# Performance work log

Measured on AMD Instinct MI355X. Metric: run time of the kernel, lower is better.

## Reference

```python
import jax, jax.numpy as jnp
import numpy as np

# H36M 17-joint skeleton: parent-of array
_PARENTS = [-1, 0, 1, 2, 0, 4, 5, 0, 7, 8, 9, 8, 11, 12, 8, 14, 15]

def _make_triplets():
    # (jp, j, jc) for every joint j with a parent jp and child jc
    trips = []
    for jc, j in enumerate(_PARENTS):
        if j <= 0 and j != 0:
            continue
        if j == -1:
            continue
        jp = _PARENTS[j]
        if jp == -1:
            continue
        trips.append((jp, j, jc))
    return trips

TRIPLETS = _make_triplets()  # 12 fixed triplets

B, N, J, C = 16, 243, 17, 512
H, D = 8, C // 8
EPS = 1e-5


def setup_inputs() -> dict:
    key = jax.random.key(0)
    ks = jax.random.split(key, 5)
    s = 1.0 / np.sqrt(C)
    x = jax.random.normal(ks[0], (B, N, J, C), dtype=jnp.float32)
    Wqkv = jax.random.normal(ks[1], (C, 3 * C), dtype=jnp.float32) * s
    bqkv = jax.random.normal(ks[2], (3 * C,), dtype=jnp.float32) * 0.01
    Wproj = jax.random.normal(ks[3], (C, C), dtype=jnp.float32) * s
    bproj = jax.random.normal(ks[4], (C,), dtype=jnp.float32) * 0.01
    return {"x": x, "Wqkv": Wqkv, "bqkv": bqkv, "Wproj": Wproj, "bproj": bproj}


def _hsdm(x, Wqkv, bqkv, Wproj, bproj):
    # x: (B, N, J, C) -> tokens over joints per frame
    xf = x.reshape(B * N, J, C)
    qkv = xf @ Wqkv + bqkv                                   # (BN, J, 3C)
    qkv = qkv.reshape(B * N, J, 3, H, D).transpose(2, 0, 3, 1, 4)  # (3, BN, H, J, D)
    q, k, v = qkv[0], qkv[1], qkv[2]
    scale = 1.0 / jnp.sqrt(jnp.float32(D))
    attn = jax.nn.softmax(jnp.einsum('bhqd,bhkd->bhqk', q, k) * scale, axis=-1)
    # sequential hierarchical adjustment over fixed skeleton triplets
    # (order matters: later triplets read entries written by earlier ones)
    for jp, j, jc in TRIPLETS:
        half = attn[:, :, j, jp] * 0.5
        attn = attn.at[:, :, j, jc].add(half).at[:, :, jc, j].add(half)
    # dropout is identity at inference
    xa = jnp.einsum('bhqk,bhkd->bhqd', attn, v)              # (BN, H, J, D)
    xa = xa.transpose(0, 2, 1, 3).reshape(B * N, J, C)
    xa = xa @ Wproj + bproj
    y = x + xa.reshape(B, N, J, C)
    mu = jnp.mean(y, axis=-1, keepdims=True)
    var = jnp.var(y, axis=-1, keepdims=True)
    return (y - mu) / jnp.sqrt(var + EPS)                     # LN without affine


def reference(x, Wqkv, bqkv, Wproj, bproj):
    return _hsdm(x, Wqkv, bqkv, Wproj, bproj)
```

## Files before the change

### kernel.cpp

```cpp
#include <hip/hip_runtime.h>

typedef unsigned short u16;
typedef unsigned int u32;
typedef short bf16x8 __attribute__((ext_vector_type(8)));
typedef float f32x4 __attribute__((ext_vector_type(4)));
typedef float f32x16 __attribute__((ext_vector_type(16)));

#define M_ROWS   66096
#define M_PAD    66176
#define C_DIM    512
#define NQKV     1536
#define NFRAME   3888


__device__ __forceinline__ u16 f2bf(float f) {
    u32 u = __float_as_uint(f);
    u32 r = (u + 0x7fffu + ((u >> 16) & 1u)) >> 16;
    return (u16)r;
}
__device__ __forceinline__ float bf2f(u16 v) {
    return __uint_as_float(((u32)v) << 16);
}
__device__ __forceinline__ void async16(const void* g, void* l) {
    __builtin_amdgcn_global_load_lds(
        (const __attribute__((address_space(1))) unsigned int*)g,
        (__attribute__((address_space(3))) unsigned int*)l, 16, 0, 0);
}


__global__ __launch_bounds__(256) void cast_x(const float* __restrict__ x, u16* __restrict__ xb) {
    u32 cid = blockIdx.x * 256u + threadIdx.x;
    u32 m  = cid >> 6;
    u32 c0 = (cid & 63u) * 8u;
    if (m >= M_PAD) return;
    u16 v[8];
    if (m < M_ROWS) {
        const float* p = x + (size_t)m * C_DIM + c0;
        float4 f1 = *(const float4*)p;
        float4 f2 = *(const float4*)(p + 4);
        v[0]=f2bf(f1.x); v[1]=f2bf(f1.y); v[2]=f2bf(f1.z); v[3]=f2bf(f1.w);
        v[4]=f2bf(f2.x); v[5]=f2bf(f2.y); v[6]=f2bf(f2.z); v[7]=f2bf(f2.w);
    } else {
        #pragma unroll
        for (int i = 0; i < 8; ++i) v[i] = 0;
    }
    u16* dst = xb + ((size_t)(c0 >> 5) * M_PAD + m) * 32 + (c0 & 31u);
    *(uint4*)dst = *(const uint4*)v;
}


__global__ __launch_bounds__(256) void cast_w(const float* __restrict__ W, u16* __restrict__ out, int N) {
    __shared__ float tile[32 * 65];
    const int n0 = blockIdx.x * 64;
    const int kt = blockIdx.y;
    const int t  = threadIdx.x;
    for (int i = t; i < 2048; i += 256) {
        int k = i >> 6, n = i & 63;
        tile[k * 65 + n] = W[(size_t)(kt * 32 + k) * N + n0 + n];
    }
    __syncthreads();
    {
        int n = t >> 2, kk0 = (t & 3) * 8;
        u16 v[8];
        #pragma unroll
        for (int j = 0; j < 8; ++j) v[j] = f2bf(tile[(kk0 + j) * 65 + n]);
        u16* dst = out + ((size_t)kt * N + n0 + n) * 32 + kk0;
        *(uint4*)dst = *(const uint4*)v;
    }
}


__global__ __launch_bounds__(256) void gemm1(const u16* __restrict__ xb,
                                             const u16* __restrict__ wt,
                                             const float* __restrict__ bqkv,
                                             u16* __restrict__ qkv) {
    __shared__ u16 As[2][128 * 32];
    __shared__ u16 Bs[2][128 * 32];
    __shared__ float biasS[128];

    const int n0 = blockIdx.x * 128;
    const int m0 = blockIdx.y * 128;
    const int t  = threadIdx.x;
    const int w  = t >> 6, l = t & 63;
    const int lr = l & 15, lq = l >> 4;
    const int wr = (w >> 1) * 64, wc = (w & 1) * 64;

    if (t < 128) biasS[t] = bqkv[n0 + t];

    f32x4 acc[4][4] = {};

    auto stage = [&](int kt, int bi) {
        const u16* ga = xb + ((size_t)kt * M_PAD + m0) * 32;
        const u16* gb = wt + ((size_t)kt * NQKV + n0) * 32;
        async16(ga + (size_t)t * 8,         &As[bi][t * 8]);
        async16(ga + (size_t)(t + 256) * 8, &As[bi][(t + 256) * 8]);
        async16(gb + (size_t)t * 8,         &Bs[bi][t * 8]);
        async16(gb + (size_t)(t + 256) * 8, &Bs[bi][(t + 256) * 8]);
    };

    stage(0, 0);
    __syncthreads();

    for (int kt = 0; kt < 16; ++kt) {
        const int cur = kt & 1;
        if (kt < 15) stage(kt + 1, cur ^ 1);

        bf16x8 a[4], b[4];
        #pragma unroll
        for (int i = 0; i < 4; ++i) a[i] = *(const bf16x8*)&As[cur][(wr + i * 16 + lr) * 32 + lq * 8];
        #pragma unroll
        for (int i = 0; i < 4; ++i) b[i] = *(const bf16x8*)&Bs[cur][(wc + i * 16 + lr) * 32 + lq * 8];
        #pragma unroll
        for (int i = 0; i < 4; ++i)
            #pragma unroll
            for (int j = 0; j < 4; ++j)
                acc[i][j] = __builtin_amdgcn_mfma_f32_16x16x32_bf16(a[i], b[j], acc[i][j], 0, 0, 0);

        __syncthreads();
    }

    #pragma unroll
    for (int i = 0; i < 4; ++i) {
        #pragma unroll
        for (int j = 0; j < 4; ++j) {
            const int col  = n0 + wc + j * 16 + lr;
            const float bb = biasS[wc + j * 16 + lr];
            #pragma unroll
            for (int r = 0; r < 4; ++r) {
                const int row = m0 + wr + i * 16 + lq * 4 + r;
                if (row < M_ROWS)
                    qkv[(size_t)row * NQKV + col] = f2bf(acc[i][j][r] + bb);
            }
        }
    }
}


__global__ __launch_bounds__(256) void attn_k(const u16* __restrict__ qkv, u16* __restrict__ xa) {
    __shared__ u16 Pb[4][32 * 40];

    const int wv  = threadIdx.x >> 6;
    const int l   = threadIdx.x & 63;
    const int l31 = l & 31;
    const int hi  = l >> 5;

    const int id = blockIdx.x * 4 + wv;
    const int f  = id >> 3;
    const int h  = id & 7;

    const int mrow = (l31 < 17) ? l31 : 0;
    const u16* base = qkv + (size_t)(f * 17) * NQKV;
    const u16* Qp = base + (size_t)mrow * NQKV + h * 64 + 8 * hi;
    const u16* Kp = Qp + 512;

    f32x16 Sacc = {};
    #pragma unroll
    for (int c = 0; c < 4; ++c) {
        bf16x8 aq = *(const bf16x8*)(Qp + 16 * c);
        bf16x8 bk = *(const bf16x8*)(Kp + 16 * c);
        Sacc = __builtin_amdgcn_mfma_f32_32x32x16_bf16(aq, bk, Sacc, 0, 0, 0);
    }

    float p[16];
    #pragma unroll
    for (int r = 0; r < 16; ++r)
        p[r] = (l31 < 17) ? Sacc[r] * 0.125f : -1e30f;

    #pragma unroll
    for (int r = 0; r < 16; ++r) {
        float mx = p[r];
        #pragma unroll
        for (int m = 1; m < 32; m <<= 1) mx = fmaxf(mx, __shfl_xor(mx, m));
        float e = __expf(p[r] - mx);
        float s = e;
        #pragma unroll
        for (int m = 1; m < 32; m <<= 1) s += __shfl_xor(s, m);
        p[r] = e * __builtin_amdgcn_rcpf(s);
    }

    {
        constexpr int TJP[13] = {0,1,0,4,0,7,8,7,8,11,7,8,14};
        constexpr int TJ [13] = {1,2,4,5,7,8,9,8,11,12,8,14,15};
        constexpr int TJC[13] = {2,3,5,6,8,9,10,11,12,13,14,15,16};
        #pragma unroll
        for (int tr = 0; tr < 13; ++tr) {
            const int jp = TJP[tr], j = TJ[tr], jc = TJC[tr];
            const int rj = (j  & 3) | ((j  >> 3) << 2), hj = (j  >> 2) & 1;
            const int rc = (jc & 3) | ((jc >> 3) << 2), hc = (jc >> 2) & 1;
            const float half = 0.5f * __shfl(p[rj], jp + 32 * hj);
            if (l == jc + 32 * hj) p[rj] += half;
            if (l == j  + 32 * hc) p[rc] += half;
        }
    }

    u16* Pw = Pb[wv];
    #pragma unroll
    for (int r = 0; r < 16; ++r) {
        const int row = (r & 3) + 8 * (r >> 2) + 4 * hi;
        Pw[row * 40 + l31] = f2bf(p[r]);
    }
    asm volatile("s_waitcnt lgkmcnt(0)" ::: "memory");

    bf16x8 pa[2];
    #pragma unroll
    for (int c = 0; c < 2; ++c)
        pa[c] = *(const bf16x8*)&Pw[l31 * 40 + 16 * c + 8 * hi];

    const u16* Vbase = base + 1024 + h * 64;
    f32x16 O[2] = {};
    #pragma unroll
    for (int t = 0; t < 2; ++t) {
        #pragma unroll
        for (int c = 0; c < 2; ++c) {
            u16 vv[8];
            #pragma unroll
            for (int j = 0; j < 8; ++j) {
                const int k  = 16 * c + 8 * hi + j;
                const int kr = (k < 17) ? k : 0;
                vv[j] = Vbase[(size_t)kr * NQKV + t * 32 + l31];
            }
            O[t] = __builtin_amdgcn_mfma_f32_32x32x16_bf16(pa[c], *(const bf16x8*)vv, O[t], 0, 0, 0);
        }
    }

    #pragma unroll
    for (int t = 0; t < 2; ++t) {
        const int kt = h * 2 + t;
        #pragma unroll
        for (int r = 0; r < 16; ++r) {
            const int row = (r & 3) + 8 * (r >> 2) + 4 * hi;
            if (row < 17)
                xa[((size_t)kt * M_PAD + (f * 17 + row)) * 32 + l31] = f2bf(O[t][r]);
        }
    }
}


__global__ __launch_bounds__(256, 4) void gemm2_ln(const u16* __restrict__ xa,
                                                   const u16* __restrict__ wt,
                                                   const float* __restrict__ bproj,
                                                   const float* __restrict__ x,
                                                   float* __restrict__ out) {
    __shared__ u16 As[2][2048];
    __shared__ float partS[32][5];
    __shared__ float partQ[32][5];

    const int m0 = blockIdx.x * 32;
    const int t  = threadIdx.x;
    const int wn = t >> 6, l = t & 63;
    const int lr = l & 15, lq = l >> 4;

    f32x4 acc[2][8] = {};

    auto stageA = [&](int s, int bi) {
        const int sub = t >> 7;
        const int idx = t & 127;
        const u16* src = xa + ((size_t)(2 * s + sub) * M_PAD + m0) * 32 + idx * 8;
        async16(src, &As[bi][sub * 1024 + idx * 8]);
    };

    stageA(0, 0);
    __syncthreads();

    for (int s = 0; s < 8; ++s) {
        const int buf = s & 1;
        if (s < 7) stageA(s + 1, buf ^ 1);

        #pragma unroll
        for (int sub = 0; sub < 2; ++sub) {
            const int kt = 2 * s + sub;
            const u16* gb = wt + ((size_t)kt * C_DIM + wn * 128 + lr) * 32 + lq * 8;
            bf16x8 a[2], b[8];
            #pragma unroll
            for (int j = 0; j < 8; ++j) b[j] = *(const bf16x8*)(gb + (size_t)j * 512);
            #pragma unroll
            for (int i = 0; i < 2; ++i)
                a[i] = *(const bf16x8*)&As[buf][sub * 1024 + (i * 16 + lr) * 32 + lq * 8];
            #pragma unroll
            for (int i = 0; i < 2; ++i)
                #pragma unroll
                for (int j = 0; j < 8; ++j)
                    acc[i][j] = __builtin_amdgcn_mfma_f32_16x16x32_bf16(a[i], b[j], acc[i][j], 0, 0, 0);
        }

        __syncthreads();
    }

    float bias_[8];
    #pragma unroll
    for (int j = 0; j < 8; ++j) bias_[j] = bproj[wn * 128 + j * 16 + lr];

    #pragma unroll
    for (int i = 0; i < 2; ++i) {
        #pragma unroll
        for (int rr = 0; rr < 4; ++rr) {
            const int rl   = i * 16 + lq * 4 + rr;
            const int rowg = m0 + rl;
            const bool valid = rowg < M_ROWS;
            const float* xr = x + (size_t)rowg * C_DIM + wn * 128 + lr;
            float s = 0.f, q = 0.f;
            #pragma unroll
            for (int j = 0; j < 8; ++j) {
                float v = acc[i][j][rr] + bias_[j];
                if (valid) v += xr[j * 16];
                acc[i][j][rr] = v;
                s += v;
                q += v * v;
            }
            #pragma unroll
            for (int m = 1; m < 16; m <<= 1) {
                s += __shfl_xor(s, m);
                q += __shfl_xor(q, m);
            }
            if (lr == 0) {
                partS[rl][wn] = s;
                partQ[rl][wn] = q;
            }
        }
    }
    __syncthreads();

    if (t < 32) {
        float ss = 0.f, qq = 0.f;
        #pragma unroll
        for (int w2 = 0; w2 < 4; ++w2) { ss += partS[t][w2]; qq += partQ[t][w2]; }
        const float mean = ss * (1.f / 512.f);
        const float var  = qq * (1.f / 512.f) - mean * mean;
        partS[t][4] = mean;
        partQ[t][4] = rsqrtf(var + 1e-5f);
    }
    __syncthreads();

    #pragma unroll
    for (int i = 0; i < 2; ++i) {
        #pragma unroll
        for (int rr = 0; rr < 4; ++rr) {
            const int rl   = i * 16 + lq * 4 + rr;
            const int rowg = m0 + rl;
            if (rowg < M_ROWS) {
                const float mean = partS[rl][4];
                const float rstd = partQ[rl][4];
                float* orow = out + (size_t)rowg * C_DIM + wn * 128 + lr;
                #pragma unroll
                for (int j = 0; j < 8; ++j)
                    orow[j * 16] = (acc[i][j][rr] - mean) * rstd;
            }
        }
    }
}


extern "C" void kernel_launch(void* const* d_in, const int* in_sizes, int n_in,
                              void* d_out, int out_size, void* d_ws, size_t ws_size,
                              hipStream_t stream) {
    const float* x     = (const float*)d_in[0];
    const float* Wqkv  = (const float*)d_in[1];
    const float* bqkv  = (const float*)d_in[2];
    const float* Wproj = (const float*)d_in[3];
    const float* bproj = (const float*)d_in[4];
    float* out = (float*)d_out;

    u16* xb  = (u16*)d_ws;
    u16* wqt = xb  + (size_t)M_PAD * C_DIM;
    u16* wpt = wqt + (size_t)NQKV * C_DIM;
    u16* qkv = wpt + (size_t)C_DIM * C_DIM;
    u16* xa  = qkv + (size_t)M_PAD * NQKV;

    cast_x<<<(M_PAD * 64) / 256, 256, 0, stream>>>(x, xb);
    cast_w<<<dim3(NQKV / 64, 16), 256, 0, stream>>>(Wqkv, wqt, NQKV);
    cast_w<<<dim3(C_DIM / 64, 16), 256, 0, stream>>>(Wproj, wpt, C_DIM);
    gemm1<<<dim3(NQKV / 128, M_PAD / 128), 256, 0, stream>>>(xb, wqt, bqkv, qkv);
    attn_k<<<(NFRAME * 8) / 4, 256, 0, stream>>>(qkv, xa);
    gemm2_ln<<<(M_PAD / 32), 256, 0, stream>>>(xa, wpt, bproj, x, out);
}
```

Baseline: 635.9 us.

## Stage each frame's QKV rows in LDS with one block per frame

The attention kernel now assigns one 512-thread block per frame, with each of the 8 waves handling one head. The block loads the frame's full 17x1536 QKV slab into LDS using coalesced 16-byte loads. Q, K and V fragments are then read from LDS instead of as scattered global loads, which were especially costly for the strided per-element V gathers. In exchange, the kernel uses about 52KB of LDS per block and adds a block-wide barrier, which limits occupancy.

New measurement: 649.8 us. 2.2% more time.

```diff
diff --git a/kernel.cpp b/kernel.cpp
--- a/kernel.cpp
+++ b/kernel.cpp
@@ -136,28 +136,43 @@
 }
 
 
-__global__ __launch_bounds__(256) void attn_k(const u16* __restrict__ qkv, u16* __restrict__ xa) {
-    __shared__ u16 Pb[4][32 * 40];
-
-    const int wv  = threadIdx.x >> 6;
-    const int l   = threadIdx.x & 63;
+#define FR_STRIDE 1544
+
+__global__ __launch_bounds__(512) void attn_k(const u16* __restrict__ qkv, u16* __restrict__ xa) {
+    __shared__ u16 Flds[17 * FR_STRIDE];
+    __shared__ u16 Pb[8][32 * 40];
+
+    const int t   = threadIdx.x;
+    const int wv  = t >> 6;
+    const int l   = t & 63;
     const int l31 = l & 31;
     const int hi  = l >> 5;
 
-    const int id = blockIdx.x * 4 + wv;
-    const int f  = id >> 3;
-    const int h  = id & 7;
+    const int f = blockIdx.x;
+    const int h = wv;
+
+    {
+        const u16* fb = qkv + (size_t)f * 17 * NQKV;
+        #pragma unroll
+        for (int i = 0; i < 7; ++i) {
+            const int c = t + i * 512;
+            if (c < 3264) {
+                const int row  = c / 192;
+                const int col8 = c - row * 192;
+                uint4 v = *(const uint4*)(fb + (size_t)row * NQKV + col8 * 8);
+                *(uint4*)&Flds[row * FR_STRIDE + col8 * 8] = v;
+            }
+        }
+    }
+    __syncthreads();
 
     const int mrow = (l31 < 17) ? l31 : 0;
-    const u16* base = qkv + (size_t)(f * 17) * NQKV;
-    const u16* Qp = base + (size_t)mrow * NQKV + h * 64 + 8 * hi;
-    const u16* Kp = Qp + 512;
 
     f32x16 Sacc = {};
     #pragma unroll
     for (int c = 0; c < 4; ++c) {
-        bf16x8 aq = *(const bf16x8*)(Qp + 16 * c);
-        bf16x8 bk = *(const bf16x8*)(Kp + 16 * c);
+        bf16x8 aq = *(const bf16x8*)&Flds[mrow * FR_STRIDE + h * 64 + 8 * hi + 16 * c];
+        bf16x8 bk = *(const bf16x8*)&Flds[mrow * FR_STRIDE + 512 + h * 64 + 8 * hi + 16 * c];
         Sacc = __builtin_amdgcn_mfma_f32_32x32x16_bf16(aq, bk, Sacc, 0, 0, 0);
     }
 
@@ -206,10 +221,9 @@
     for (int c = 0; c < 2; ++c)
         pa[c] = *(const bf16x8*)&Pw[l31 * 40 + 16 * c + 8 * hi];
 
-    const u16* Vbase = base + 1024 + h * 64;
     f32x16 O[2] = {};
     #pragma unroll
-    for (int t = 0; t < 2; ++t) {
+    for (int t2 = 0; t2 < 2; ++t2) {
         #pragma unroll
         for (int c = 0; c < 2; ++c) {
             u16 vv[8];
@@ -217,20 +231,20 @@
             for (int j = 0; j < 8; ++j) {
                 const int k  = 16 * c + 8 * hi + j;
                 const int kr = (k < 17) ? k : 0;
-                vv[j] = Vbase[(size_t)kr * NQKV + t * 32 + l31];
-            }
-            O[t] = __builtin_amdgcn_mfma_f32_32x32x16_bf16(pa[c], *(const bf16x8*)vv, O[t], 0, 0, 0);
-        }
-    }
-
-    #pragma unroll
-    for (int t = 0; t < 2; ++t) {
-        const int kt = h * 2 + t;
+                vv[j] = Flds[kr * FR_STRIDE + 1024 + h * 64 + t2 * 32 + l31];
+            }
+            O[t2] = __builtin_amdgcn_mfma_f32_32x32x16_bf16(pa[c], *(const bf16x8*)vv, O[t2], 0, 0, 0);
+        }
+    }
+
+    #pragma unroll
+    for (int t2 = 0; t2 < 2; ++t2) {
+        const int kt = h * 2 + t2;
         #pragma unroll
         for (int r = 0; r < 16; ++r) {
             const int row = (r & 3) + 8 * (r >> 2) + 4 * hi;
             if (row < 17)
-                xa[((size_t)kt * M_PAD + (f * 17 + row)) * 32 + l31] = f2bf(O[t][r]);
+                xa[((size_t)kt * M_PAD + (f * 17 + row)) * 32 + l31] = f2bf(O[t2][r]);
         }
     }
 }
@@ -370,6 +384,6 @@
     cast_w<<<dim3(NQKV / 64, 16), 256, 0, stream>>>(Wqkv, wqt, NQKV);
     cast_w<<<dim3(C_DIM / 64, 16), 256, 0, stream>>>(Wproj, wpt, C_DIM);
     gemm1<<<dim3(NQKV / 128, M_PAD / 128), 256, 0, stream>>>(xb, wqt, bqkv, qkv);
-    attn_k<<<(NFRAME * 8) / 4, 256, 0, stream>>>(qkv, xa);
+    attn_k<<<NFRAME, 512, 0, stream>>>(qkv, xa);
     gemm2_ln<<<(M_PAD / 32), 256, 0, stream>>>(xa, wpt, bproj, x, out);
 }
```
